# Optimization experiments

Measured on AMD Instinct MI355X. Metric: run time of the kernel, lower is better.

The kernel has to match this reference:

```python
import jax, jax.numpy as jnp
import numpy as np

K_S = 2  # spatial order
K_T = 3  # temporal localization factor


def setup_inputs() -> dict:
    key = jax.random.key(0)
    ks = jax.random.split(key, 5)
    B, T, N = 8, 12, 250
    return {
        "history_data": jax.random.normal(ks[0], (B, T, N, 128), dtype=jnp.float32),
        "Prior": jax.random.normal(ks[1], (B, T, N, 64), dtype=jnp.float32),
        "Observed": jax.random.normal(ks[2], (B, T, N, 32), dtype=jnp.float32),
        "W_emb": jax.random.normal(ks[3], (224, 64), dtype=jnp.float32) * 0.05,
        "b_emb": jnp.zeros((64,), dtype=jnp.float32),
        "use_X": 1,
    }


def _transition(adj):
    # P = D^{-1} A : faithful to diag-embed @ adj, realized as row scaling
    rowsum = adj.sum(axis=-1) + 1e-9
    d_inv = 1.0 / rowsum
    d_inv = jnp.where(jnp.isinf(d_inv) | jnp.isnan(d_inv), 0.0, d_inv)
    return d_inv[..., :, None] * adj


def _forward(history_data, Prior, Observed, W_emb, b_emb):
    # nodevec: [B,T,N,64]
    nodevec = jnp.tanh(
        jnp.concatenate([history_data, Prior, Observed], axis=-1) @ W_emb + b_emb
    )
    # similarity: [B,T,N,N]
    sim = jax.nn.relu(jnp.einsum("btnd,btmd->btnm", nodevec, nodevec))
    # symmetric normalization D^{-1/2} S D^{-1/2}
    d = (sim.sum(axis=-1) + 1e-9) ** -0.5
    adj = d[..., :, None] * sim * d[..., None, :]
    P1 = jnp.swapaxes(_transition(adj), -2, -1)
    P2 = jnp.swapaxes(_transition(jnp.swapaxes(adj, -2, -1)), -2, -1)
    N = adj.shape[-1]
    mask = 1.0 - jnp.eye(N, dtype=adj.dtype)
    outs = []
    for g in (P1, P2):
        k1 = g
        ordered = [k1 * mask]
        for _k in range(2, K_S + 1):
            k1 = k1 @ g
            ordered.append(k1 * mask)
        for og in ordered:
            B, T, Nn, _ = og.shape
            # st_localization: tile each row K_T times along last dim
            ex = jnp.broadcast_to(og[..., None, :], (B, T, Nn, K_T, Nn))
            outs.append(ex.reshape(B, T, Nn, K_T * Nn))
    return tuple(outs)


def reference(history_data, Prior, Observed, W_emb, b_emb, use_X):
    # use_X == 1 path (fc_x_emb on concatenated features)
    return _forward(history_data, Prior, Observed, W_emb, b_emb)
```

## Files before the change

kernel.cpp:

```cpp
#include <hip/hip_runtime.h>
#include <hip/hip_bf16.h>

#define G_N 96
#define N_N 250
#define N_P 256
#define E_N 64
#define OUT_GSTRIDE (250 * 750)
#define OUT_STRIDE  (96 * 250 * 750)

typedef __attribute__((ext_vector_type(4))) float floatx4;
typedef __attribute__((ext_vector_type(2))) float floatx2;
typedef __attribute__((ext_vector_type(8))) short shortx8;
typedef __attribute__((ext_vector_type(4))) short shortx4;

__device__ __forceinline__ float bf2f(unsigned short u) {
    union { unsigned int i; float f; } v; v.i = ((unsigned int)u) << 16; return v.f;
}
__device__ __forceinline__ unsigned short f2bf(float f) {
    union { float f; unsigned int i; } v; v.f = f;
    unsigned int x = v.i;
    return (unsigned short)((x + 0x7fffu + ((x >> 16) & 1u)) >> 16);
}

__global__ __launch_bounds__(256) void k_embed(
    const float* __restrict__ hist, const float* __restrict__ prior,
    const float* __restrict__ obs, const float* __restrict__ Wemb,
    const float* __restrict__ bemb, unsigned short* __restrict__ nvb)
{
    __shared__ __attribute__((aligned(16))) float Xt[32][68];
    __shared__ __attribute__((aligned(16))) float Wl[32][64];
    const int t  = threadIdx.x;
    const int tx = t & 15, ty = t >> 4;
    const int rr0 = blockIdx.x * 64;
    const int g   = rr0 >> 8;
    const int n0  = rr0 & 255;

    float acc[4][4] = {};

    for (int c = 0; c < 7; ++c) {
        const float* src; int rowlen, off;
        if (c < 4)      { src = hist;  rowlen = 128; off = c << 5; }
        else if (c < 6) { src = prior; rowlen = 64;  off = (c - 4) << 5; }
        else            { src = obs;   rowlen = 32;  off = 0; }
        __syncthreads();
        {
            const int d  = t & 31;
            const int nb = t >> 5;
            #pragma unroll
            for (int p = 0; p < 8; ++p) {
                const int nl = nb + p * 8;
                const int n  = n0 + nl;
                float v = 0.0f;
                if (n < N_N) v = src[(size_t)(g * N_N + n) * rowlen + off + d];
                Xt[d][nl] = v;
            }
        }
        {
            const int e  = t & 63;
            const int db = t >> 6;
            #pragma unroll
            for (int p = 0; p < 8; ++p) {
                const int dl = db + p * 4;
                Wl[dl][e] = Wemb[(c * 32 + dl) * 64 + e];
            }
        }
        __syncthreads();
        #pragma unroll
        for (int k = 0; k < 32; ++k) {
            const float4 av = *(const float4*)&Xt[k][4 * ty];
            const float4 bv = *(const float4*)&Wl[k][4 * tx];
            const float a[4] = {av.x, av.y, av.z, av.w};
            const float b[4] = {bv.x, bv.y, bv.z, bv.w};
            #pragma unroll
            for (int r = 0; r < 4; ++r)
                #pragma unroll
                for (int cc = 0; cc < 4; ++cc)
                    acc[r][cc] = fmaf(a[r], b[cc], acc[r][cc]);
        }
    }
    #pragma unroll
    for (int r = 0; r < 4; ++r) {
        const int nl = 4 * ty + r;
        const int n  = n0 + nl;
        unsigned short* d2 = nvb + ((size_t)g * N_P + (n0 + nl)) * E_N + 4 * tx;
        #pragma unroll
        for (int cc = 0; cc < 4; ++cc) {
            float v = 0.0f;
            if (n < N_N) v = tanhf(acc[r][cc] + bemb[4 * tx + cc]);
            d2[cc] = f2bf(v);
        }
    }
}

__global__ __launch_bounds__(256) void k_sim(
    const unsigned short* __restrict__ nvb, unsigned short* __restrict__ Sb,
    float* __restrict__ rowsum)
{
    const int blk = blockIdx.x;
    const int g   = blk >> 4;
    const int i0  = (blk & 15) << 4;
    const int t    = threadIdx.x;
    const int w    = t >> 6;
    const int lane = t & 63;
    const int m = lane & 15, kg = lane >> 4;

    const shortx8* nvg = (const shortx8*)(nvb + (size_t)g * N_P * E_N);
    const shortx8 a0 = nvg[(i0 + m) * 8 + kg];
    const shortx8 a1 = nvg[(i0 + m) * 8 + 4 + kg];

    floatx4 acc[4];
    const floatx4 zero = {0.f, 0.f, 0.f, 0.f};
    #pragma unroll
    for (int tt = 0; tt < 4; ++tt) {
        const int j = (w << 6) + (tt << 4) + m;
        const shortx8 b0 = nvg[j * 8 + kg];
        const shortx8 b1 = nvg[j * 8 + 4 + kg];
        floatx4 c = zero;
        c = __builtin_amdgcn_mfma_f32_16x16x32_bf16(a0, b0, c, 0, 0, 0);
        c = __builtin_amdgcn_mfma_f32_16x16x32_bf16(a1, b1, c, 0, 0, 0);
        acc[tt] = c;
    }

    float v[4] = {0.f, 0.f, 0.f, 0.f};
    unsigned short* Sg = Sb + (size_t)g * N_P * N_P;
    #pragma unroll
    for (int tt = 0; tt < 4; ++tt) {
        #pragma unroll
        for (int r = 0; r < 4; ++r) {
            float s = acc[tt][r];
            s = s > 0.f ? s : 0.f;
            const int il = (kg << 2) + r;
            const int j  = (w << 6) + (tt << 4) + m;
            Sg[(size_t)(i0 + il) * N_P + j] = f2bf(s);
            v[r] += s;
        }
    }
    #pragma unroll
    for (int r = 0; r < 4; ++r) {
        v[r] += __shfl_xor(v[r], 1);
        v[r] += __shfl_xor(v[r], 2);
        v[r] += __shfl_xor(v[r], 4);
        v[r] += __shfl_xor(v[r], 8);
    }
    __shared__ float rs[4][16];
    if (m == 0) {
        #pragma unroll
        for (int r = 0; r < 4; ++r) rs[w][(kg << 2) + r] = v[r];
    }
    __syncthreads();
    if (t < 16) rowsum[g * N_P + i0 + t] = rs[0][t] + rs[1][t] + rs[2][t] + rs[3][t];
}

__global__ __launch_bounds__(256) void k_trans(
    const unsigned short* __restrict__ Sb, const float* __restrict__ rowsum,
    float* __restrict__ cArr, float* __restrict__ wArr)
{
    const int blk = (blockIdx.x & 7) * 768 + (blockIdx.x >> 3);
    const int g  = blk >> 6;
    const int r0 = (blk & 63) << 2;
    const int t = threadIdx.x;
    const int w = t >> 6, lane = t & 63;
    __shared__ __attribute__((aligned(16))) float dL[N_P];
    dL[t] = rsqrtf(rowsum[g * N_P + t] + 1e-9f);
    __syncthreads();
    const int row = r0 + w;
    const shortx4 sv = *(const shortx4*)(Sb + (size_t)g * N_P * N_P
                                         + (size_t)row * N_P + lane * 4);
    const float4 dv = *(const float4*)&dL[lane * 4];
    float a = bf2f((unsigned short)sv[0]) * dv.x
            + bf2f((unsigned short)sv[1]) * dv.y
            + bf2f((unsigned short)sv[2]) * dv.z
            + bf2f((unsigned short)sv[3]) * dv.w;
    #pragma unroll
    for (int s = 32; s; s >>= 1) a += __shfl_xor(a, s);
    if (lane == 0) {
        const float d = dL[row];
        const float r = 1.0f / (d * a + 1e-9f);
        const float c = r * d;
        cArr[g * N_P + row] = c;
        wArr[g * N_P + row] = c * d;
    }
}

__global__ __launch_bounds__(256) void k_pq(
    const unsigned short* __restrict__ Sb, const float* __restrict__ rowsum,
    const float* __restrict__ cArr, const float* __restrict__ wArr,
    float* __restrict__ out)
{
    const int blk = (blockIdx.x & 7) * 192 + (blockIdx.x >> 3);
    const int g   = blk >> 4;
    const int i0  = (blk & 15) << 4;
    const int t    = threadIdx.x;
    const int w    = t >> 6;
    const int lane = t & 63;
    const int m = lane & 15, kg = lane >> 4;

    __shared__ __attribute__((aligned(16))) unsigned short As[16][40];
    __shared__ __attribute__((aligned(16))) unsigned short Bs[256][40];
    __shared__ __attribute__((aligned(16))) float wL[N_P];
    __shared__ __attribute__((aligned(16))) float cC[N_P];
    __shared__ float dR16[16];

    wL[t] = wArr[g * N_P + t];
    cC[t] = cArr[g * N_P + t];
    if (t < 16) dR16[t] = rsqrtf(rowsum[g * N_P + i0 + t] + 1e-9f);

    const unsigned short* Sg = Sb + (size_t)g * N_P * N_P;

    floatx4 acc[4];
    const floatx4 zero = {0.f, 0.f, 0.f, 0.f};
    #pragma unroll
    for (int tt = 0; tt < 4; ++tt) acc[tt] = zero;

    for (int kb = 0; kb < 8; ++kb) {
        __syncthreads();
        if (t < 64) {
            const int row = t >> 2, c4 = t & 3;
            *(uint4*)&As[row][c4 * 8] =
                *(const uint4*)(Sg + (size_t)(i0 + row) * N_P + kb * 32 + c4 * 8);
        }
        #pragma unroll
        for (int q4 = 0; q4 < 4; ++q4) {
            const int u = t + (q4 << 8);
            const int row = u >> 2, c4 = u & 3;
            *(uint4*)&Bs[row][c4 * 8] =
                *(const uint4*)(Sg + (size_t)row * N_P + kb * 32 + c4 * 8);
        }
        __syncthreads();
        const shortx8 a = *(const shortx8*)&As[m][kg << 3];
        const float4 w0 = *(const float4*)&wL[kb * 32 + (kg << 3)];
        const float4 w1 = *(const float4*)&wL[kb * 32 + (kg << 3) + 4];
        const float wv[8] = {w0.x, w0.y, w0.z, w0.w, w1.x, w1.y, w1.z, w1.w};
        shortx8 aw;
        #pragma unroll
        for (int u = 0; u < 8; ++u)
            aw[u] = (short)f2bf(bf2f((unsigned short)a[u]) * wv[u]);
        #pragma unroll
        for (int tt = 0; tt < 4; ++tt) {
            const shortx8 b = *(const shortx8*)&Bs[(w << 6) + (tt << 4) + m][kg << 3];
            acc[tt] = __builtin_amdgcn_mfma_f32_16x16x32_bf16(aw, b, acc[tt], 0, 0, 0);
        }
    }

    float* o1 = out + (size_t)OUT_STRIDE     + (size_t)g * OUT_GSTRIDE;
    float* o3 = out + 3 * (size_t)OUT_STRIDE + (size_t)g * OUT_GSTRIDE;
    const float dRq[4] = {dR16[(kg << 2)], dR16[(kg << 2) + 1],
                          dR16[(kg << 2) + 2], dR16[(kg << 2) + 3]};
    #pragma unroll
    for (int tt = 0; tt < 4; ++tt) {
        const int J = (w << 6) + (tt << 4) + m;
        if (J < N_N) {
            const float cj = cC[J];
            #pragma unroll
            for (int r = 0; r < 4; ++r) {
                const int I = i0 + (kg << 2) + r;
                if (I < N_N) {
                    const float qv = (I == J) ? 0.f : acc[tt][r] * dRq[r] * cj;
                    float* b1 = o1 + (size_t)I * 750 + J;
                    float* b3 = o3 + (size_t)I * 750 + J;
                    b1[0] = qv; b1[250] = qv; b1[500] = qv;
                    b3[0] = qv; b3[250] = qv; b3[500] = qv;
                }
            }
        }
    }

    float* o0 = out + (size_t)g * OUT_GSTRIDE;
    float* o2 = o0 + 2 * (size_t)OUT_STRIDE;
    const int c0 = lane << 2;
    #pragma unroll
    for (int rr = 0; rr < 4; ++rr) {
        const int row = (rr << 2) + w;
        const int i   = i0 + row;
        if (i >= N_N) continue;
        if (c0 >= 252) continue;
        const float dI = dR16[row];
        const shortx4 sv = *(const shortx4*)(Sg + (size_t)i * N_P + c0);
        const float4 cc4 = *(const float4*)&cC[c0];
        float p0 = (i == c0)     ? 0.f : dI * bf2f((unsigned short)sv[0]) * cc4.x;
        float p1 = (i == c0 + 1) ? 0.f : dI * bf2f((unsigned short)sv[1]) * cc4.y;
        float p2 = (i == c0 + 2) ? 0.f : dI * bf2f((unsigned short)sv[2]) * cc4.z;
        float p3 = (i == c0 + 3) ? 0.f : dI * bf2f((unsigned short)sv[3]) * cc4.w;
        const floatx2 pxy = {p0, p1}, pzw = {p2, p3};
        float* b0 = o0 + (size_t)i * 750 + c0;
        float* b2 = o2 + (size_t)i * 750 + c0;
        #pragma unroll
        for (int rep = 0; rep < 3; ++rep) {
            const int o = rep * 250;
            *(floatx2*)(b0 + o) = pxy;
            *(floatx2*)(b2 + o) = pxy;
            if (c0 < 246) {
                *(floatx2*)(b0 + o + 2) = pzw;
                *(floatx2*)(b2 + o + 2) = pzw;
            }
        }
    }
}

extern "C" void kernel_launch(void* const* d_in, const int* in_sizes, int n_in,
                              void* d_out, int out_size, void* d_ws, size_t ws_size,
                              hipStream_t stream) {
    const float* hist  = (const float*)d_in[0];
    const float* prior = (const float*)d_in[1];
    const float* obs   = (const float*)d_in[2];
    const float* Wemb  = (const float*)d_in[3];
    const float* bemb  = (const float*)d_in[4];
    float* out = (float*)d_out;

    char* p = (char*)d_ws;
    unsigned short* nvb = (unsigned short*)p; p += (size_t)G_N * N_P * E_N * 2;
    unsigned short* Sb  = (unsigned short*)p; p += (size_t)G_N * N_P * N_P * 2;
    float* rowsum = (float*)p; p += (size_t)G_N * N_P * 4;
    float* cArr   = (float*)p; p += (size_t)G_N * N_P * 4;
    float* wArr   = (float*)p; p += (size_t)G_N * N_P * 4;

    k_embed<<<dim3(G_N * N_P / 64), dim3(256), 0, stream>>>(hist, prior, obs, Wemb, bemb, nvb);
    k_sim  <<<dim3(G_N * 16),       dim3(256), 0, stream>>>(nvb, Sb, rowsum);
    k_trans<<<dim3(G_N * 64),       dim3(256), 0, stream>>>(Sb, rowsum, cArr, wArr);
    k_pq   <<<dim3(G_N * 16),       dim3(256), 0, stream>>>(Sb, rowsum, cArr, wArr, out);
}
```

Before: 442.6 us.

## Load MFMA operands directly from global and stage Q output through LDS

Removes the per-k-block LDS staging of the A and B tiles in k_pq, so MFMA operands are read directly from global/L2 and the two barriers per iteration are dropped. The Q result is written into an LDS tile, then stored with the same coalesced vectorized float2 pattern as the P outputs instead of scattered scalar stores. It also adds a minimum-occupancy hint to launch_bounds. The cost is redundant global loads of B rows across waves and blocks, plus an extra barrier and LDS round trip for the epilogue.

```diff
diff --git a/kernel.cpp b/kernel.cpp
--- a/kernel.cpp
+++ b/kernel.cpp
@@ -182,7 +182,7 @@
     }
 }
 
-__global__ __launch_bounds__(256) void k_pq(
+__global__ __launch_bounds__(256, 4) void k_pq(
     const unsigned short* __restrict__ Sb, const float* __restrict__ rowsum,
     const float* __restrict__ cArr, const float* __restrict__ wArr,
     float* __restrict__ out)
@@ -195,15 +195,15 @@
     const int lane = t & 63;
     const int m = lane & 15, kg = lane >> 4;
 
-    __shared__ __attribute__((aligned(16))) unsigned short As[16][40];
-    __shared__ __attribute__((aligned(16))) unsigned short Bs[256][40];
     __shared__ __attribute__((aligned(16))) float wL[N_P];
     __shared__ __attribute__((aligned(16))) float cC[N_P];
     __shared__ float dR16[16];
+    __shared__ __attribute__((aligned(16))) float qAll[16][260];
 
     wL[t] = wArr[g * N_P + t];
     cC[t] = cArr[g * N_P + t];
     if (t < 16) dR16[t] = rsqrtf(rowsum[g * N_P + i0 + t] + 1e-9f);
+    __syncthreads();
 
     const unsigned short* Sg = Sb + (size_t)g * N_P * N_P;
 
@@ -212,24 +212,13 @@
     #pragma unroll
     for (int tt = 0; tt < 4; ++tt) acc[tt] = zero;
 
+    const unsigned short* aRow = Sg + (size_t)(i0 + m) * N_P + (kg << 3);
+    #pragma unroll 2
     for (int kb = 0; kb < 8; ++kb) {
-        __syncthreads();
-        if (t < 64) {
-            const int row = t >> 2, c4 = t & 3;
-            *(uint4*)&As[row][c4 * 8] =
-                *(const uint4*)(Sg + (size_t)(i0 + row) * N_P + kb * 32 + c4 * 8);
-        }
-        #pragma unroll
-        for (int q4 = 0; q4 < 4; ++q4) {
-            const int u = t + (q4 << 8);
-            const int row = u >> 2, c4 = u & 3;
-            *(uint4*)&Bs[row][c4 * 8] =
-                *(const uint4*)(Sg + (size_t)row * N_P + kb * 32 + c4 * 8);
-        }
-        __syncthreads();
-        const shortx8 a = *(const shortx8*)&As[m][kg << 3];
-        const float4 w0 = *(const float4*)&wL[kb * 32 + (kg << 3)];
-        const float4 w1 = *(const float4*)&wL[kb * 32 + (kg << 3) + 4];
+        const int k0 = kb * 32;
+        const shortx8 a = *(const shortx8*)(aRow + k0);
+        const float4 w0 = *(const float4*)&wL[k0 + (kg << 3)];
+        const float4 w1 = *(const float4*)&wL[k0 + (kg << 3) + 4];
         const float wv[8] = {w0.x, w0.y, w0.z, w0.w, w1.x, w1.y, w1.z, w1.w};
         shortx8 aw;
         #pragma unroll
@@ -237,42 +226,35 @@
             aw[u] = (short)f2bf(bf2f((unsigned short)a[u]) * wv[u]);
         #pragma unroll
         for (int tt = 0; tt < 4; ++tt) {
-            const shortx8 b = *(const shortx8*)&Bs[(w << 6) + (tt << 4) + m][kg << 3];
+            const int j = (w << 6) + (tt << 4) + m;
+            const shortx8 b = *(const shortx8*)(Sg + (size_t)j * N_P + k0 + (kg << 3));
             acc[tt] = __builtin_amdgcn_mfma_f32_16x16x32_bf16(aw, b, acc[tt], 0, 0, 0);
         }
     }
 
-    float* o1 = out + (size_t)OUT_STRIDE     + (size_t)g * OUT_GSTRIDE;
-    float* o3 = out + 3 * (size_t)OUT_STRIDE + (size_t)g * OUT_GSTRIDE;
-    const float dRq[4] = {dR16[(kg << 2)], dR16[(kg << 2) + 1],
-                          dR16[(kg << 2) + 2], dR16[(kg << 2) + 3]};
     #pragma unroll
     for (int tt = 0; tt < 4; ++tt) {
-        const int J = (w << 6) + (tt << 4) + m;
-        if (J < N_N) {
-            const float cj = cC[J];
-            #pragma unroll
-            for (int r = 0; r < 4; ++r) {
-                const int I = i0 + (kg << 2) + r;
-                if (I < N_N) {
-                    const float qv = (I == J) ? 0.f : acc[tt][r] * dRq[r] * cj;
-                    float* b1 = o1 + (size_t)I * 750 + J;
-                    float* b3 = o3 + (size_t)I * 750 + J;
-                    b1[0] = qv; b1[250] = qv; b1[500] = qv;
-                    b3[0] = qv; b3[250] = qv; b3[500] = qv;
-                }
-            }
-        }
-    }
+        #pragma unroll
+        for (int r = 0; r < 4; ++r) {
+            const int lrow = (kg << 2) + r;
+            const int col  = (w << 6) + (tt << 4) + m;
+            float qv = acc[tt][r] * dR16[lrow] * cC[col];
+            if (i0 + lrow == col) qv = 0.f;
+            qAll[lrow][col] = qv;
+        }
+    }
+    __syncthreads();
 
     float* o0 = out + (size_t)g * OUT_GSTRIDE;
+    float* o1 = o0 + (size_t)OUT_STRIDE;
     float* o2 = o0 + 2 * (size_t)OUT_STRIDE;
+    float* o3 = o0 + 3 * (size_t)OUT_STRIDE;
     const int c0 = lane << 2;
-    #pragma unroll
     for (int rr = 0; rr < 4; ++rr) {
         const int row = (rr << 2) + w;
         const int i   = i0 + row;
         if (i >= N_N) continue;
+        const floatx4 q4 = *(const floatx4*)&qAll[row][c0 & 252];
         if (c0 >= 252) continue;
         const float dI = dR16[row];
         const shortx4 sv = *(const shortx4*)(Sg + (size_t)i * N_P + c0);
@@ -282,16 +264,23 @@
         float p2 = (i == c0 + 2) ? 0.f : dI * bf2f((unsigned short)sv[2]) * cc4.z;
         float p3 = (i == c0 + 3) ? 0.f : dI * bf2f((unsigned short)sv[3]) * cc4.w;
         const floatx2 pxy = {p0, p1}, pzw = {p2, p3};
+        const floatx2 qxy = {q4[0], q4[1]}, qzw = {q4[2], q4[3]};
         float* b0 = o0 + (size_t)i * 750 + c0;
+        float* b1 = o1 + (size_t)i * 750 + c0;
         float* b2 = o2 + (size_t)i * 750 + c0;
+        float* b3 = o3 + (size_t)i * 750 + c0;
         #pragma unroll
         for (int rep = 0; rep < 3; ++rep) {
             const int o = rep * 250;
             *(floatx2*)(b0 + o) = pxy;
+            *(floatx2*)(b1 + o) = qxy;
             *(floatx2*)(b2 + o) = pxy;
-            if (c0 < 246) {
+            *(floatx2*)(b3 + o) = qxy;
+            if (lane < 62) {
                 *(floatx2*)(b0 + o + 2) = pzw;
+                *(floatx2*)(b1 + o + 2) = qzw;
                 *(floatx2*)(b2 + o + 2) = pzw;
+                *(floatx2*)(b3 + o + 2) = qzw;
             }
         }
     }
```

Result: faster. 394.9 us (-10.8%).
